# Kernel optimization log

Hardware: AMD Instinct MI355X
Metric: run time of the kernel (lower is better)

## Reference

```python
import jax, jax.numpy as jnp
import numpy as np


def setup_inputs() -> dict:
    key = jax.random.key(0)
    k1, k2 = jax.random.split(key)
    N_NODES, MAX_DEGREE, BATCH = 100000, 128, 262144
    # adj_info: padded adjacency lists, entries are node ids in [0, N_NODES)
    adj_info = jax.random.randint(k1, (N_NODES, MAX_DEGREE), 0, N_NODES, dtype=jnp.int32)
    ids = jax.random.randint(k2, (BATCH,), 0, N_NODES, dtype=jnp.int32)
    return {"adj_info": adj_info, "ids": ids, "num_samples": 25}


def reference(adj_info, ids, num_samples):
    # embedding_lookup: gather adjacency rows -> [B, max_degree]
    adj_lists = jnp.take(adj_info, ids, axis=0)
    # weights are a copy of the adjacency entries in the original module
    # tf.random_shuffle on the transposed [D, B] tensor permutes the neighbor
    # axis with a SINGLE permutation shared across all rows.
    max_degree = adj_lists.shape[1]
    perm = jax.random.permutation(jax.random.key(42), max_degree)
    shuffled = adj_lists[:, perm]                  # [B, max_degree]
    adj_sampled = shuffled[:, :num_samples]        # slice first num_samples
    weights_sampled = shuffled[:, :num_samples]
    return adj_sampled, weights_sampled
```

## Files before the change

### kernel.cpp

```cpp
#include <hip/hip_runtime.h>
#include <algorithm>
#include <cstdint>


static inline void threefry2x32_block(uint32_t k0, uint32_t k1,
                                      uint32_t& x0, uint32_t& x1) {
  auto rotl = [](uint32_t v, int d) { return (v << d) | (v >> (32 - d)); };
  const int r0[4] = {13, 15, 26, 6};
  const int r1[4] = {17, 29, 16, 24};
  const uint32_t ks0 = k0, ks1 = k1, ks2 = k0 ^ k1 ^ 0x1BD11BDAu;
  x0 += ks0; x1 += ks1;
  for (int i = 0; i < 4; ++i) { x0 += x1; x1 = rotl(x1, r0[i]); x1 ^= x0; }
  x0 += ks1; x1 += ks2 + 1u;
  for (int i = 0; i < 4; ++i) { x0 += x1; x1 = rotl(x1, r1[i]); x1 ^= x0; }
  x0 += ks2; x1 += ks0 + 2u;
  for (int i = 0; i < 4; ++i) { x0 += x1; x1 = rotl(x1, r0[i]); x1 ^= x0; }
  x0 += ks0; x1 += ks1 + 3u;
  for (int i = 0; i < 4; ++i) { x0 += x1; x1 = rotl(x1, r1[i]); x1 ^= x0; }
  x0 += ks1; x1 += ks2 + 4u;
  for (int i = 0; i < 4; ++i) { x0 += x1; x1 = rotl(x1, r0[i]); x1 ^= x0; }
  x0 += ks2; x1 += ks0 + 5u;
}

struct Perm25 { int p[25]; };

static Perm25 compute_perm25() {
  uint32_t sk0 = 0u, sk1 = 1u;
  threefry2x32_block(0u, 42u, sk0, sk1);

  uint32_t bits[128];
  for (int i = 0; i < 128; ++i) {
    uint32_t x0 = 0u, x1 = (uint32_t)i;
    threefry2x32_block(sk0, sk1, x0, x1);
    bits[i] = x0 ^ x1;
  }

  int idxs[128];
  for (int i = 0; i < 128; ++i) idxs[i] = i;
  std::stable_sort(idxs, idxs + 128,
                   [&](int a, int b) { return bits[a] < bits[b]; });

  Perm25 out;
  for (int j = 0; j < 25; ++j) out.p[j] = idxs[j];
  return out;
}


#define NS 25
#define MAX_DEG 128
#define ROWS_PER_BLOCK 32
#define LDS_STRIDE 132
#define ELEMS (ROWS_PER_BLOCK * NS)

__global__ __launch_bounds__(256)
void uniform_sampler_kernel(const int* __restrict__ adj,
                            const int* __restrict__ ids,
                            int* __restrict__ out,
                            Perm25 perm, int batch) {
  __shared__ int s_rows[ROWS_PER_BLOCK * LDS_STRIDE];
  __shared__ int s_ids[ROWS_PER_BLOCK];
  __shared__ int s_perm[NS];

  const int tid = threadIdx.x;
  const int row0 = blockIdx.x * ROWS_PER_BLOCK;

  if (tid < ROWS_PER_BLOCK) {
    const int gr = row0 + tid;
    s_ids[tid] = (gr < batch) ? ids[gr] : 0;
  }
  if (tid < NS) s_perm[tid] = perm.p[tid];
  __syncthreads();

#pragma unroll
  for (int it = 0; it < 4; ++it) {
    const int r = it * 8 + (tid >> 5);
    const int c = tid & 31;
    const int node = s_ids[r];
    const int4 v =
        *reinterpret_cast<const int4*>(adj + (size_t)node * MAX_DEG + c * 4);
    *reinterpret_cast<int4*>(&s_rows[r * LDS_STRIDE + c * 4]) = v;
  }
  __syncthreads();

  if (tid < ELEMS / 4) {
    int vals[4];
#pragma unroll
    for (int e = 0; e < 4; ++e) {
      const int li = tid * 4 + e;
      const unsigned r = (unsigned)li / NS;
      const int j = li - (int)r * NS;
      vals[e] = s_rows[r * LDS_STRIDE + s_perm[j]];
    }
    const int4 v = make_int4(vals[0], vals[1], vals[2], vals[3]);
    const size_t base = (size_t)blockIdx.x * ELEMS + (size_t)tid * 4;
    const size_t total = (size_t)batch * NS;
    if (base + 4 <= total) {
      *reinterpret_cast<int4*>(out + base) = v;
      *reinterpret_cast<int4*>(out + total + base) = v;
    }
  }
}

extern "C" void kernel_launch(void* const* d_in, const int* in_sizes, int n_in,
                              void* d_out, int out_size, void* d_ws, size_t ws_size,
                              hipStream_t stream) {
  const int* adj = (const int*)d_in[0];
  const int* ids = (const int*)d_in[1];

  const int batch = in_sizes[1];

  const Perm25 perm = compute_perm25();

  const int grid = (batch + ROWS_PER_BLOCK - 1) / ROWS_PER_BLOCK;
  uniform_sampler_kernel<<<grid, 256, 0, stream>>>(adj, ids, (int*)d_out,
                                                   perm, batch);
}
```

Measured before the change: 32.08 us.

## Precompact permuted neighbor columns per node, then gather compact rows per batch

Adds a first kernel that reads every adjacency row once and writes the 25 permuted sampled columns into a compact 32-int workspace table. A second kernel then gathers 128-byte compact rows per batch id instead of full 512-byte rows, and writes outputs with nontemporal stores. The aim is to cut redundant gather traffic, since the batch is larger than the node count and ids repeat. In exchange it adds a second kernel launch and a full pass over all nodes, and it depends on having enough workspace, falling back to the direct kernel otherwise.

```diff
diff --git a/kernel.cpp b/kernel.cpp
--- a/kernel.cpp
+++ b/kernel.cpp
@@ -27,50 +27,133 @@
 static Perm25 compute_perm25() {
   uint32_t sk0 = 0u, sk1 = 1u;
   threefry2x32_block(0u, 42u, sk0, sk1);
-
   uint32_t bits[128];
   for (int i = 0; i < 128; ++i) {
     uint32_t x0 = 0u, x1 = (uint32_t)i;
     threefry2x32_block(sk0, sk1, x0, x1);
     bits[i] = x0 ^ x1;
   }
-
   int idxs[128];
   for (int i = 0; i < 128; ++i) idxs[i] = i;
   std::stable_sort(idxs, idxs + 128,
                    [&](int a, int b) { return bits[a] < bits[b]; });
-
   Perm25 out;
   for (int j = 0; j < 25; ++j) out.p[j] = idxs[j];
   return out;
 }
-
 
 #define NS 25
 #define MAX_DEG 128
 #define ROWS_PER_BLOCK 32
 #define LDS_STRIDE 132
+#define TMP_STRIDE 32
 #define ELEMS (ROWS_PER_BLOCK * NS)
 
+typedef int iv4 __attribute__((ext_vector_type(4)));
+
 __global__ __launch_bounds__(256)
-void uniform_sampler_kernel(const int* __restrict__ adj,
-                            const int* __restrict__ ids,
-                            int* __restrict__ out,
-                            Perm25 perm, int batch) {
+void compact_rows_kernel(const int* __restrict__ adj,
+                         int* __restrict__ tmp,
+                         Perm25 perm, int n_nodes) {
+  __shared__ int s_rows[ROWS_PER_BLOCK * LDS_STRIDE];
+  __shared__ int s_perm[NS];
+
+  const int tid = threadIdx.x;
+  const int row0 = blockIdx.x * ROWS_PER_BLOCK;
+  if (tid < NS) s_perm[tid] = perm.p[tid];
+  __syncthreads();
+
+#pragma unroll
+  for (int it = 0; it < 4; ++it) {
+    const int r = it * 8 + (tid >> 5);
+    const int c = tid & 31;
+    const int node = row0 + r;
+    if (node < n_nodes) {
+      const int4 v =
+          *reinterpret_cast<const int4*>(adj + (size_t)node * MAX_DEG + c * 4);
+      *reinterpret_cast<int4*>(&s_rows[r * LDS_STRIDE + c * 4]) = v;
+    }
+  }
+  __syncthreads();
+
+  const int r = tid >> 3;
+  const int q = tid & 7;
+  const int node = row0 + r;
+  if (node < n_nodes) {
+    iv4 v;
+#pragma unroll
+    for (int e = 0; e < 4; ++e) {
+      const int j = q * 4 + e;
+      v[e] = (j < NS) ? s_rows[r * LDS_STRIDE + s_perm[j]] : 0;
+    }
+    *reinterpret_cast<iv4*>(tmp + (size_t)node * TMP_STRIDE + q * 4) = v;
+  }
+}
+
+#define B_STRIDE 36
+
+__global__ __launch_bounds__(256)
+void scatter_out_kernel(const int* __restrict__ tmp,
+                        const int* __restrict__ ids,
+                        int* __restrict__ out, int batch) {
+  __shared__ int s_tmp[ROWS_PER_BLOCK * B_STRIDE];
+  __shared__ int s_ids[ROWS_PER_BLOCK];
+
+  const int tid = threadIdx.x;
+  const int row0 = blockIdx.x * ROWS_PER_BLOCK;
+
+  if (tid < ROWS_PER_BLOCK) {
+    const int gr = row0 + tid;
+    s_ids[tid] = (gr < batch) ? ids[gr] : 0;
+  }
+  __syncthreads();
+
+  {
+    const int r = tid >> 3;
+    const int q = tid & 7;
+    const int node = s_ids[r];
+    const int4 v = *reinterpret_cast<const int4*>(
+        tmp + (size_t)node * TMP_STRIDE + q * 4);
+    *reinterpret_cast<int4*>(&s_tmp[r * B_STRIDE + q * 4]) = v;
+  }
+  __syncthreads();
+
+  if (tid < ELEMS / 4) {
+    iv4 v;
+#pragma unroll
+    for (int e = 0; e < 4; ++e) {
+      const int li = tid * 4 + e;
+      const unsigned r = (unsigned)li / NS;
+      const int j = li - (int)r * NS;
+      v[e] = s_tmp[r * B_STRIDE + j];
+    }
+    const size_t base = (size_t)blockIdx.x * ELEMS + (size_t)tid * 4;
+    const size_t total = (size_t)batch * NS;
+    if (base + 4 <= total) {
+      __builtin_nontemporal_store(v, reinterpret_cast<iv4*>(out + base));
+      __builtin_nontemporal_store(v,
+                                  reinterpret_cast<iv4*>(out + total + base));
+    }
+  }
+}
+
+__global__ __launch_bounds__(256)
+void direct_sampler_kernel(const int* __restrict__ adj,
+                           const int* __restrict__ ids,
+                           int* __restrict__ out,
+                           Perm25 perm, int batch) {
   __shared__ int s_rows[ROWS_PER_BLOCK * LDS_STRIDE];
   __shared__ int s_ids[ROWS_PER_BLOCK];
   __shared__ int s_perm[NS];
 
   const int tid = threadIdx.x;
   const int row0 = blockIdx.x * ROWS_PER_BLOCK;
-
   if (tid < ROWS_PER_BLOCK) {
     const int gr = row0 + tid;
     s_ids[tid] = (gr < batch) ? ids[gr] : 0;
   }
   if (tid < NS) s_perm[tid] = perm.p[tid];
   __syncthreads();
-
 #pragma unroll
   for (int it = 0; it < 4; ++it) {
     const int r = it * 8 + (tid >> 5);
@@ -81,22 +164,21 @@
     *reinterpret_cast<int4*>(&s_rows[r * LDS_STRIDE + c * 4]) = v;
   }
   __syncthreads();
-
   if (tid < ELEMS / 4) {
-    int vals[4];
+    iv4 v;
 #pragma unroll
     for (int e = 0; e < 4; ++e) {
       const int li = tid * 4 + e;
       const unsigned r = (unsigned)li / NS;
       const int j = li - (int)r * NS;
-      vals[e] = s_rows[r * LDS_STRIDE + s_perm[j]];
-    }
-    const int4 v = make_int4(vals[0], vals[1], vals[2], vals[3]);
+      v[e] = s_rows[r * LDS_STRIDE + s_perm[j]];
+    }
     const size_t base = (size_t)blockIdx.x * ELEMS + (size_t)tid * 4;
     const size_t total = (size_t)batch * NS;
     if (base + 4 <= total) {
-      *reinterpret_cast<int4*>(out + base) = v;
-      *reinterpret_cast<int4*>(out + total + base) = v;
+      __builtin_nontemporal_store(v, reinterpret_cast<iv4*>(out + base));
+      __builtin_nontemporal_store(v,
+                                  reinterpret_cast<iv4*>(out + total + base));
     }
   }
 }
@@ -107,11 +189,21 @@
   const int* adj = (const int*)d_in[0];
   const int* ids = (const int*)d_in[1];
 
+  const int n_nodes = in_sizes[0] / MAX_DEG;
   const int batch = in_sizes[1];
 
   const Perm25 perm = compute_perm25();
 
-  const int grid = (batch + ROWS_PER_BLOCK - 1) / ROWS_PER_BLOCK;
-  uniform_sampler_kernel<<<grid, 256, 0, stream>>>(adj, ids, (int*)d_out,
-                                                   perm, batch);
-}
+  const size_t tmp_bytes = (size_t)n_nodes * TMP_STRIDE * sizeof(int);
+  const int gridB = (batch + ROWS_PER_BLOCK - 1) / ROWS_PER_BLOCK;
+
+  if (ws_size >= tmp_bytes) {
+    int* tmp = (int*)d_ws;
+    const int gridA = (n_nodes + ROWS_PER_BLOCK - 1) / ROWS_PER_BLOCK;
+    compact_rows_kernel<<<gridA, 256, 0, stream>>>(adj, tmp, perm, n_nodes);
+    scatter_out_kernel<<<gridB, 256, 0, stream>>>(tmp, ids, (int*)d_out, batch);
+  } else {
+    direct_sampler_kernel<<<gridB, 256, 0, stream>>>(adj, ids, (int*)d_out,
+                                                     perm, batch);
+  }
+}
```

After: 28.65 us. -10.7%, faster.
